# Optimization experiments

Measured on AMD Instinct MI355X. Metric: run time of the kernel, lower is better.

## Reference

```python
import jax, jax.numpy as jnp
import numpy as np

N = 4096
D_IN = 3000
D_HID = 512
D_OUT = 64
NEG_SLOPE = 0.2  # LeakyReLU alpha used by GraphAttentionLayer(.., 0.2, 0.2)
MASK_FILL = -9e15


def setup_inputs() -> dict:
    key = jax.random.key(0)
    ks = jax.random.split(key, 13)

    def p(k, shape, fan_in):
        return jax.random.normal(k, shape, dtype=jnp.float32) * np.float32(1.0 / np.sqrt(fan_in))

    return {
        "features_omics1": jax.random.normal(ks[0], (N, D_IN), dtype=jnp.float32),
        "feat_adj_omics1": jax.random.randint(ks[1], (N, N), 0, 2, dtype=jnp.int32),
        "spatial_adj_omics1": jax.random.randint(ks[2], (N, N), 0, 2, dtype=jnp.int32),
        # encoder_1: GAT(D_IN -> D_HID); encoder_2: GAT(D_HID -> D_OUT)
        "W_enc1": p(ks[3], (D_IN, D_HID), D_IN),
        "a_enc1": p(ks[4], (2 * D_HID, 1), D_HID),
        "W_enc2": p(ks[5], (D_HID, D_OUT), D_HID),
        "a_enc2": p(ks[6], (2 * D_OUT, 1), D_OUT),
        # decoder_1: GAT(D_OUT -> D_HID); decoder_2: GAT(D_HID -> D_IN)
        "W_dec1": p(ks[7], (D_OUT, D_HID), D_OUT),
        "a_dec1": p(ks[8], (2 * D_HID, 1), D_HID),
        "W_dec2": p(ks[9], (D_HID, D_IN), D_HID),
        "a_dec2": p(ks[10], (2 * D_IN, 1), D_IN),
        # AttentionLayer fusion over the two views
        "w_omega": p(ks[11], (D_OUT, D_OUT), D_OUT),
        "u_omega": p(ks[12], (D_OUT, 1), D_OUT),
    }


def _gat(h, adj, W, a):
    """Canonical dense-adjacency GAT layer (pyGAT), dropout off, ELU output."""
    Wh = h @ W                                   # [N, F]
    f = W.shape[1]
    # e[i,j] = leaky_relu(a1.Wh_i + a2.Wh_j)
    e = jax.nn.leaky_relu(Wh @ a[:f] + (Wh @ a[f:]).T, NEG_SLOPE)  # [N, N]
    att = jax.nn.softmax(jnp.where(adj > 0, e, MASK_FILL), axis=1)
    return jax.nn.elu(att @ Wh)


def _encode(x, adj, W1, a1, W2, a2):
    return _gat(_gat(x, adj, W1, a1), adj, W2, a2)


def _att_fuse(e1, e2, w_omega, u_omega):
    emb = jnp.stack([e1, e2], axis=1)            # [N, 2, D]
    v = jnp.tanh(emb @ w_omega)                  # [N, 2, D]
    vu = (v @ u_omega)[..., 0]                   # [N, 2]
    alpha = jax.nn.softmax(vu + 1e-6, axis=1)    # [N, 2]
    fused = jnp.einsum('nkd,nk->nd', emb, alpha)
    return fused, alpha


def reference(features_omics1, feat_adj_omics1, spatial_adj_omics1,
              W_enc1, a_enc1, W_enc2, a_enc2,
              W_dec1, a_dec1, W_dec2, a_dec2,
              w_omega, u_omega):
    feat_emb = _encode(features_omics1, feat_adj_omics1, W_enc1, a_enc1, W_enc2, a_enc2)
    sp_emb = _encode(features_omics1, spatial_adj_omics1, W_enc1, a_enc1, W_enc2, a_enc2)
    emb_latent, alpha = _att_fuse(feat_emb, sp_emb, w_omega, u_omega)
    recon = _gat(_gat(emb_latent, spatial_adj_omics1, W_dec1, a_dec1),
                 spatial_adj_omics1, W_dec2, a_dec2)
    corr_f = _encode(recon, feat_adj_omics1, W_enc1, a_enc1, W_enc2, a_enc2)
    corr_s = _encode(recon, spatial_adj_omics1, W_enc1, a_enc1, W_enc2, a_enc2)
    corr, _ = _att_fuse(corr_f, corr_s, w_omega, u_omega)
    return emb_latent, recon, corr, alpha
```

## Files before the change

kernel.cpp:

```cpp
#include <hip/hip_runtime.h>
#include <hip/hip_bf16.h>
#include <math.h>

using u16 = unsigned short;
using u32 = unsigned int;

typedef __attribute__((ext_vector_type(8))) short s8v;
typedef __attribute__((ext_vector_type(4))) float f4v;

__device__ __forceinline__ float bf2f(u16 u) {
    u32 x = ((u32)u) << 16;
    return __builtin_bit_cast(float, x);
}
__device__ __forceinline__ u16 f2bf(float f) {
    u32 x = __builtin_bit_cast(u32, f);
    x += 0x7fffu + ((x >> 16) & 1u);
    return (u16)(x >> 16);
}

__device__ __forceinline__ f4v mfma_bf16(s8v a, s8v b, f4v c) {
    return __builtin_amdgcn_mfma_f32_16x16x32_bf16(a, b, c, 0, 0, 0);
}

#define GLL(srcp, dstp) __builtin_amdgcn_global_load_lds( \
    (const __attribute__((address_space(1))) void*)(srcp), \
    (__attribute__((address_space(3))) void*)(dstp), 16, 0, 0)

__device__ __forceinline__ void xcd_swz(int& bx, int& by, int& bz) {
    const int nx = gridDim.x, ny = gridDim.y;
    const int total = nx * ny * gridDim.z;
    int i = (bz * ny + by) * nx + bx;
    const int q = total >> 3, r = total & 7;
    const int xcd = i & 7, k = i >> 3;
    int j = ((xcd < r) ? xcd * (q + 1) : r * (q + 1) + (xcd - r) * q) + k;
    bx = j % nx; j /= nx;
    by = j % ny;
    bz = j / ny;
}

template<bool DO_ELU, bool OUT_F32, bool OUT_SPLIT>
__global__ __launch_bounds__(256) void tgemm(
    const u16* __restrict__ A, const u16* __restrict__ Bt,
    void* __restrict__ Cv, int M, int N, int K,
    u16* __restrict__ Sh, u16* __restrict__ Sl, int Cp)
{
    constexpr int BM = 128, BN = 64, BK = 64;
    __shared__ __align__(16) u16 As[2][BM * BK];
    __shared__ __align__(16) u16 Bs[2][BN * BK];

    int bx = blockIdx.x, by = blockIdx.y, bz = blockIdx.z;
    xcd_swz(bx, by, bz);
    const int bm0 = by * BM, bn0 = bx * BN;
    const int tid = threadIdx.x;
    const int lane = tid & 63;
    const int wave = tid >> 6;
    const int wr = wave >> 1, wc = wave & 1;
    const int lr = lane & 15;
    const int srow = lane >> 3, schk = lane & 7;

    f4v acc[4][2] = {};

    auto stage = [&](int buf, int k0) {
#pragma unroll
        for (int ci = 0; ci < 4; ci++) {
            const int r8 = (wave * 4 + ci) * 8;
            const int row = r8 + srow;
            const int gchk = schk ^ (row & 7);
            GLL(A + (size_t)(bm0 + row) * K + k0 + gchk * 8, &As[buf][r8 * 64]);
        }
#pragma unroll
        for (int ci = 0; ci < 2; ci++) {
            const int r8 = (wave * 2 + ci) * 8;
            const int row = r8 + srow;
            int gn = bn0 + row;
            if (gn >= N) gn = N - 1;
            const int gchk = schk ^ (row & 7);
            GLL(Bt + (size_t)gn * K + k0 + gchk * 8, &Bs[buf][r8 * 64]);
        }
    };

    stage(0, 0);
    __syncthreads();
    int cur = 0;
    for (int k0 = 0; k0 < K; k0 += BK) {
        if (k0 + BK < K) stage(cur ^ 1, k0 + BK);
#pragma unroll
        for (int kk = 0; kk < 2; kk++) {
            const int cbase = (lane >> 4) + kk * 4;
            s8v a[4], b[2];
#pragma unroll
            for (int m = 0; m < 4; m++) {
                const int row = wr * 64 + m * 16 + lr;
                a[m] = *(const s8v*)&As[cur][row * 64 + (cbase ^ (row & 7)) * 8];
            }
#pragma unroll
            for (int n = 0; n < 2; n++) {
                const int row = wc * 32 + n * 16 + lr;
                b[n] = *(const s8v*)&Bs[cur][row * 64 + (cbase ^ (row & 7)) * 8];
            }
#pragma unroll
            for (int m = 0; m < 4; m++)
#pragma unroll
                for (int n = 0; n < 2; n++)
                    acc[m][n] = mfma_bf16(a[m], b[n], acc[m][n]);
        }
        __syncthreads();
        cur ^= 1;
    }

#pragma unroll
    for (int m = 0; m < 4; m++)
#pragma unroll
        for (int n = 0; n < 2; n++)
#pragma unroll
            for (int i = 0; i < 4; i++) {
                int gm = bm0 + wr * 64 + m * 16 + (lane >> 4) * 4 + i;
                int gn = bn0 + wc * 32 + n * 16 + lr;
                if (gm < M && gn < N) {
                    float val = acc[m][n][i];
                    if (DO_ELU) val = val > 0.f ? val : expm1f(val);
                    if (OUT_F32) {
                        ((float*)Cv)[(size_t)gm * N + gn] = val;
                        if (OUT_SPLIT) {
                            u16 hv = f2bf(val);
                            Sh[(size_t)gm * Cp + gn] = hv;
                            Sl[(size_t)gm * Cp + gn] = f2bf(val - bf2f(hv));
                        }
                    } else {
                        ((u16*)Cv)[(size_t)gm * N + gn] = f2bf(val);
                    }
                }
            }
}

__global__ __launch_bounds__(256) void tgemm_skd(
    const u16* __restrict__ A, const u16* __restrict__ BtA,
    const u16* __restrict__ BtB, float* __restrict__ P,
    int M, int Mh, int N, int K, int KS)
{
    constexpr int BM = 128, BN = 64, BK = 64;
    __shared__ __align__(16) u16 As[2][BM * BK];
    __shared__ __align__(16) u16 Bs[2][BN * BK];

    int bx = blockIdx.x, by = blockIdx.y, kz = blockIdx.z;
    xcd_swz(bx, by, kz);
    const int bm0 = by * BM, bn0 = bx * BN;
    const u16* Bt = (bm0 < Mh) ? BtA : BtB;
    const int tid = threadIdx.x;
    const int lane = tid & 63;
    const int wave = tid >> 6;
    const int wr = wave >> 1, wc = wave & 1;
    const int lr = lane & 15;
    const int srow = lane >> 3, schk = lane & 7;

    f4v acc[4][2] = {};

    auto stage = [&](int buf, int k0) {
#pragma unroll
        for (int ci = 0; ci < 4; ci++) {
            const int r8 = (wave * 4 + ci) * 8;
            const int row = r8 + srow;
            const int gchk = schk ^ (row & 7);
            GLL(A + (size_t)(bm0 + row) * K + k0 + gchk * 8, &As[buf][r8 * 64]);
        }
#pragma unroll
        for (int ci = 0; ci < 2; ci++) {
            const int r8 = (wave * 2 + ci) * 8;
            const int row = r8 + srow;
            int gn = bn0 + row;
            if (gn >= N) gn = N - 1;
            const int gchk = schk ^ (row & 7);
            GLL(Bt + (size_t)gn * K + k0 + gchk * 8, &Bs[buf][r8 * 64]);
        }
    };

    const int kbeg = kz * KS, kend = kbeg + KS;
    stage(0, kbeg);
    __syncthreads();
    int cur = 0;
    for (int k0 = kbeg; k0 < kend; k0 += BK) {
        if (k0 + BK < kend) stage(cur ^ 1, k0 + BK);
#pragma unroll
        for (int kk = 0; kk < 2; kk++) {
            const int cbase = (lane >> 4) + kk * 4;
            s8v a[4], b[2];
#pragma unroll
            for (int m = 0; m < 4; m++) {
                const int row = wr * 64 + m * 16 + lr;
                a[m] = *(const s8v*)&As[cur][row * 64 + (cbase ^ (row & 7)) * 8];
            }
#pragma unroll
            for (int n = 0; n < 2; n++) {
                const int row = wc * 32 + n * 16 + lr;
                b[n] = *(const s8v*)&Bs[cur][row * 64 + (cbase ^ (row & 7)) * 8];
            }
#pragma unroll
            for (int m = 0; m < 4; m++)
#pragma unroll
                for (int n = 0; n < 2; n++)
                    acc[m][n] = mfma_bf16(a[m], b[n], acc[m][n]);
        }
        __syncthreads();
        cur ^= 1;
    }

    float* Pz = P + (size_t)kz * M * N;
#pragma unroll
    for (int m = 0; m < 4; m++)
#pragma unroll
        for (int n = 0; n < 2; n++)
#pragma unroll
            for (int i = 0; i < 4; i++) {
                int gm = bm0 + wr * 64 + m * 16 + (lane >> 4) * 4 + i;
                int gn = bn0 + wc * 32 + n * 16 + lr;
                if (gm < M && gn < N)
                    Pz[(size_t)gm * N + gn] = acc[m][n][i];
            }
}

template<bool ELU>
__global__ __launch_bounds__(256) void skred_kernel(
    const float* __restrict__ P, u16* __restrict__ out, int total, int sk)
{
    int i = blockIdx.x * 256 + threadIdx.x;
    if (i >= total) return;
    float s = 0.f;
    for (int z = 0; z < sk; z++) s += P[(size_t)z * total + i];
    if (ELU) s = s > 0.f ? s : expm1f(s);
    out[i] = f2bf(s);
}

template<bool ASP, bool SK>
__global__ __launch_bounds__(256) void tgemm2(
    const u16* __restrict__ A0, const u16* __restrict__ A1,
    const u16* __restrict__ Bt0, const u16* __restrict__ Bt1,
    void* __restrict__ Cv, int M, int N, int K, int KS)
{
    constexpr int BM = 128, BN = 64, BK = 32;
    __shared__ __align__(16) u16 As0[2][BM * BK];
    __shared__ __align__(16) u16 As1[ASP ? 2 : 1][ASP ? BM * BK : 8];
    __shared__ __align__(16) u16 Bs0[2][BN * BK];
    __shared__ __align__(16) u16 Bs1[2][BN * BK];

    int bx = blockIdx.x, by = blockIdx.y, kz = blockIdx.z;
    xcd_swz(bx, by, kz);
    const int bm0 = by * BM, bn0 = bx * BN;
    const int tid = threadIdx.x;
    const int lane = tid & 63;
    const int wave = tid >> 6;
    const int wr = wave >> 1, wc = wave & 1;
    const int lr = lane & 15;
    const int srow = lane >> 2;
    const int schk = lane & 3;

    auto swzr = [](int row) { return (row & 3) ^ ((row >> 2) & 1); };

    f4v acc[4][2] = {};

    auto stage = [&](int buf, int k0) {
#pragma unroll
        for (int ci = 0; ci < 2; ci++) {
            const int r16 = (wave * 2 + ci) * 16;
            const int row = r16 + srow;
            const int gchk = schk ^ swzr(row);
            const size_t goff = (size_t)(bm0 + row) * K + k0 + gchk * 8;
            GLL(A0 + goff, &As0[buf][r16 * 32]);
            if constexpr (ASP) GLL(A1 + goff, &As1[buf][r16 * 32]);
        }
        {
            const int r16 = wave * 16;
            const int row = r16 + srow;
            int gn = bn0 + row;
            if (gn >= N) gn = N - 1;
            const int gchk = schk ^ swzr(row);
            const size_t goff = (size_t)gn * K + k0 + gchk * 8;
            GLL(Bt0 + goff, &Bs0[buf][r16 * 32]);
            GLL(Bt1 + goff, &Bs1[buf][r16 * 32]);
        }
    };

    const int kbeg = SK ? kz * KS : 0;
    const int kend = SK ? kbeg + KS : K;
    stage(0, kbeg);
    __syncthreads();
    int cur = 0;
    for (int k0 = kbeg; k0 < kend; k0 += BK) {
        if (k0 + BK < kend) stage(cur ^ 1, k0 + BK);
        {
            const int cbase = lane >> 4;
            s8v a0[4], a1[ASP ? 4 : 1], b0[2], b1[2];
#pragma unroll
            for (int m = 0; m < 4; m++) {
                const int row = wr * 64 + m * 16 + lr;
                const int o = row * 32 + (cbase ^ swzr(row)) * 8;
                a0[m] = *(const s8v*)&As0[cur][o];
                if constexpr (ASP) a1[m] = *(const s8v*)&As1[cur][o];
            }
#pragma unroll
            for (int n = 0; n < 2; n++) {
                const int row = wc * 32 + n * 16 + lr;
                const int o = row * 32 + (cbase ^ swzr(row)) * 8;
                b0[n] = *(const s8v*)&Bs0[cur][o];
                b1[n] = *(const s8v*)&Bs1[cur][o];
            }
#pragma unroll
            for (int m = 0; m < 4; m++)
#pragma unroll
                for (int n = 0; n < 2; n++) {
                    acc[m][n] = mfma_bf16(a0[m], b0[n], acc[m][n]);
                    acc[m][n] = mfma_bf16(a0[m], b1[n], acc[m][n]);
                    if constexpr (ASP) acc[m][n] = mfma_bf16(a1[m], b0[n], acc[m][n]);
                }
        }
        __syncthreads();
        cur ^= 1;
    }

#pragma unroll
    for (int m = 0; m < 4; m++)
#pragma unroll
        for (int n = 0; n < 2; n++)
#pragma unroll
            for (int i = 0; i < 4; i++) {
                int gm = bm0 + wr * 64 + m * 16 + (lane >> 4) * 4 + i;
                int gn = bn0 + wc * 32 + n * 16 + lr;
                if (gm < M && gn < N) {
                    if (SK) ((float*)Cv)[(size_t)kz * M * N + (size_t)gm * N + gn] = acc[m][n][i];
                    else    ((u16*)Cv)[(size_t)gm * N + gn] = f2bf(acc[m][n][i]);
                }
            }
}

__global__ __launch_bounds__(256) void skredTS_kernel(
    const float* __restrict__ P, const float* __restrict__ a,
    u16* __restrict__ wh, u16* __restrict__ tA, u16* __restrict__ tB,
    float* __restrict__ s1, float* __restrict__ s2, int n, int sk)
{
    __shared__ u16 lds[64][72];
    const int rowbase = blockIdx.x * 64;
    const int t = threadIdx.x;
    const int rl = t >> 2, cg = t & 3;
    const int row = rowbase + rl;
    const size_t M2 = (size_t)2 * n;

    float v[16];
#pragma unroll
    for (int k = 0; k < 16; k++) v[k] = 0.f;
    for (int z = 0; z < sk; z++) {
        const float4* p = (const float4*)&P[((size_t)z * M2 + row) * 64 + cg * 16];
#pragma unroll
        for (int q = 0; q < 4; q++) {
            float4 x = p[q];
            v[q * 4 + 0] += x.x; v[q * 4 + 1] += x.y;
            v[q * 4 + 2] += x.z; v[q * 4 + 3] += x.w;
        }
    }
    u16 w[16];
    float p1 = 0.f, p2 = 0.f;
#pragma unroll
    for (int k = 0; k < 16; k++) {
        w[k] = f2bf(v[k]);
        float vr = bf2f(w[k]);
        int f = cg * 16 + k;
        p1 += vr * a[f];
        p2 += vr * a[64 + f];
    }
    *(s8v*)&wh[(size_t)row * 64 + cg * 16]     = *(s8v*)&w[0];
    *(s8v*)&wh[(size_t)row * 64 + cg * 16 + 8] = *(s8v*)&w[8];
    *(s8v*)&lds[rl][cg * 16]     = *(s8v*)&w[0];
    *(s8v*)&lds[rl][cg * 16 + 8] = *(s8v*)&w[8];

    p1 += __shfl_down(p1, 1); p1 += __shfl_down(p1, 2);
    p2 += __shfl_down(p2, 1); p2 += __shfl_down(p2, 2);
    if (cg == 0) { s1[row] = p1; s2[row] = p2; }
    __syncthreads();

    const bool hb = rowbase >= n;
    u16* tX = hb ? tB : tA;
    const int grow = rowbase - (hb ? n : 0);
    u16 o[16];
#pragma unroll
    for (int k = 0; k < 16; k++) o[k] = lds[cg * 16 + k][rl];
    *(s8v*)&tX[(size_t)rl * n + grow + cg * 16]     = *(s8v*)&o[0];
    *(s8v*)&tX[(size_t)rl * n + grow + cg * 16 + 8] = *(s8v*)&o[8];
}

__global__ __launch_bounds__(256) void splitA_kernel(
    const float* __restrict__ src, u16* __restrict__ hi, u16* __restrict__ lo,
    int C, int Cp)
{
    int r = blockIdx.y;
    int c = blockIdx.x * 256 + threadIdx.x;
    if (c >= Cp) return;
    float v = (c < C) ? src[(size_t)r * C + c] : 0.f;
    u16 h = f2bf(v);
    hi[(size_t)r * Cp + c] = h;
    lo[(size_t)r * Cp + c] = f2bf(v - bf2f(h));
}

__global__ __launch_bounds__(256) void splitBT_kernel(
    const float* __restrict__ src, u16* __restrict__ hi, u16* __restrict__ lo,
    int R, int C, int Rp)
{
    __shared__ float t[32][33];
    const int r0 = blockIdx.y * 32, c0 = blockIdx.x * 32;
    const int tr = threadIdx.x >> 5, tc = threadIdx.x & 31;
#pragma unroll
    for (int i = 0; i < 4; i++) {
        int r = r0 + tr + i * 8, c = c0 + tc;
        t[tr + i * 8][tc] = (r < R && c < C) ? src[(size_t)r * C + c] : 0.f;
    }
    __syncthreads();
#pragma unroll
    for (int i = 0; i < 4; i++) {
        int c = c0 + tr + i * 8, r = r0 + tc;
        if (c < C && r < Rp) {
            float v = t[tc][tr + i * 8];
            u16 h = f2bf(v);
            hi[(size_t)c * Rp + r] = h;
            lo[(size_t)c * Rp + r] = f2bf(v - bf2f(h));
        }
    }
}

__global__ __launch_bounds__(256) void tr_kernel(
    const u16* __restrict__ src, u16* __restrict__ dst, int R, int C)
{
    __shared__ u16 t[32][33];
    const int r0 = blockIdx.y * 32, c0 = blockIdx.x * 32;
    const int tr = threadIdx.x >> 5, tc = threadIdx.x & 31;
#pragma unroll
    for (int i = 0; i < 4; i++) {
        int r = r0 + tr + i * 8, c = c0 + tc;
        t[tr + i * 8][tc] = (r < R && c < C) ? src[(size_t)r * C + c] : (u16)0;
    }
    __syncthreads();
#pragma unroll
    for (int i = 0; i < 4; i++) {
        int c = c0 + tr + i * 8, r = r0 + tc;
        if (c < C && r < R) dst[(size_t)c * R + r] = t[tc][tr + i * 8];
    }
}

__device__ __forceinline__ float block_sum4(float v, float* red) {
#pragma unroll
    for (int off = 32; off; off >>= 1) v += __shfl_down(v, off);
    int w = threadIdx.x >> 6;
    if ((threadIdx.x & 63) == 0) red[w] = v;
    __syncthreads();
    float r = red[0] + red[1] + red[2] + red[3];
    __syncthreads();
    return r;
}
__device__ __forceinline__ float block_max4(float v, float* red) {
#pragma unroll
    for (int off = 32; off; off >>= 1) v = fmaxf(v, __shfl_down(v, off));
    int w = threadIdx.x >> 6;
    if ((threadIdx.x & 63) == 0) red[w] = v;
    __syncthreads();
    float r = fmaxf(fmaxf(red[0], red[1]), fmaxf(red[2], red[3]));
    __syncthreads();
    return r;
}

__global__ __launch_bounds__(256) void scores_kernel(
    const u16* __restrict__ Wh, int ld, int F, const float* __restrict__ a,
    float* __restrict__ s1, float* __restrict__ s2)
{
    __shared__ float red[4];
    int i = blockIdx.x, tid = threadIdx.x;
    float acc1 = 0.f, acc2 = 0.f;
    for (int f = tid; f < F; f += 256) {
        float w = bf2f(Wh[(size_t)i * ld + f]);
        acc1 += w * a[f];
        acc2 += w * a[F + f];
    }
    acc1 = block_sum4(acc1, red);
    acc2 = block_sum4(acc2, red);
    if (tid == 0) { s1[i] = acc1; s2[i] = acc2; }
}

__device__ __forceinline__ void att_row(
    const u32* mask, const float* s1, const float* s2, int soff,
    u16* att, int i, int n, float* red)
{
    int tid = threadIdx.x;
    float s1i = s1[soff + i];
    int j0 = tid * 16;
    u32 w = mask[(size_t)i * (n >> 5) + (j0 >> 5)];
    u32 bits = (j0 & 16) ? (w >> 16) : (w & 0xFFFFu);

    float e[16];
    float mx = -3.0e38f;
#pragma unroll
    for (int t = 0; t < 16; t++) {
        float x = s1i + s2[soff + j0 + t];
        x = x > 0.f ? x : 0.2f * x;
        e[t] = x;
        if ((bits >> t) & 1u) mx = fmaxf(mx, x);
    }
    mx = block_max4(mx, red);

    float sum = 0.f;
#pragma unroll
    for (int t = 0; t < 16; t++) {
        float pv = ((bits >> t) & 1u) ? expf(e[t] - mx) : 0.f;
        e[t] = pv;
        sum += pv;
    }
    sum = block_sum4(sum, red);
    float rinv = sum > 0.f ? 1.f / sum : 0.f;
#pragma unroll
    for (int t = 0; t < 16; t++)
        att[(size_t)i * n + j0 + t] = f2bf(e[t] * rinv);
}

__global__ __launch_bounds__(256) void att_kernel(
    const u32* __restrict__ mask, const float* __restrict__ s1,
    const float* __restrict__ s2, u16* __restrict__ att, int n)
{
    __shared__ float red[4];
    att_row(mask, s1, s2, 0, att, blockIdx.x, n, red);
}

__global__ __launch_bounds__(256) void att2_kernel(
    const u32* __restrict__ maskA, const u32* __restrict__ maskB,
    const float* __restrict__ s1, const float* __restrict__ s2, int offB,
    u16* __restrict__ attA, u16* __restrict__ attB, int n)
{
    __shared__ float red[4];
    int b = blockIdx.x;
    if (b < n) att_row(maskA, s1, s2, 0, attA, b, n, red);
    else      att_row(maskB, s1, s2, offB, attB, b - n, n, red);
}

__global__ __launch_bounds__(64) void fuse_kernel(
    const u16* __restrict__ E1, const u16* __restrict__ E2,
    const float* __restrict__ W, const float* __restrict__ U,
    float* __restrict__ fused, float* __restrict__ alpha,
    u16* __restrict__ eh, u16* __restrict__ el)
{
    __shared__ float e1[64], e2[64];
    int i = blockIdx.x, d = threadIdx.x;
    e1[d] = bf2f(E1[i * 64 + d]);
    e2[d] = bf2f(E2[i * 64 + d]);
    __syncthreads();
    float v1 = 0.f, v2 = 0.f;
#pragma unroll 8
    for (int f = 0; f < 64; f++) {
        float w = W[f * 64 + d];
        v1 += e1[f] * w;
        v2 += e2[f] * w;
    }
    v1 = tanhf(v1); v2 = tanhf(v2);
    float u = U[d];
    float p1 = v1 * u, p2 = v2 * u;
#pragma unroll
    for (int off = 32; off; off >>= 1) {
        p1 += __shfl_down(p1, off);
        p2 += __shfl_down(p2, off);
    }
    p1 = __shfl(p1, 0); p2 = __shfl(p2, 0);
    float m = fmaxf(p1, p2);
    float w1 = expf(p1 - m), w2 = expf(p2 - m);
    float a1 = w1 / (w1 + w2), a2 = w2 / (w1 + w2);
    float fv = a1 * e1[d] + a2 * e2[d];
    fused[i * 64 + d] = fv;
    if (eh != nullptr) {
        u16 hv = f2bf(fv);
        eh[i * 64 + d] = hv;
        el[i * 64 + d] = f2bf(fv - bf2f(hv));
    }
    if (alpha != nullptr && d < 2) alpha[i * 2 + d] = (d == 0 ? a1 : a2);
}

__global__ void bitpack_kernel(const int* __restrict__ adj,
                               u32* __restrict__ mask, int nwords)
{
    int w = blockIdx.x * 256 + threadIdx.x;
    if (w >= nwords) return;
    const int* src = adj + (size_t)w * 32;
    u32 m = 0;
#pragma unroll
    for (int b = 0; b < 32; b++) m |= (src[b] > 0 ? 1u : 0u) << b;
    mask[w] = m;
}

extern "C" void kernel_launch(void* const* d_in, const int* in_sizes, int n_in,
                              void* d_out, int out_size, void* d_ws, size_t ws_size,
                              hipStream_t stream)
{
    const int N = 4096, DIN = 3000, DINP = 3008, DH = 512, DO = 64;
    const float* x      = (const float*)d_in[0];
    const int*   adjF   = (const int*)d_in[1];
    const int*   adjS   = (const int*)d_in[2];
    const float* We1    = (const float*)d_in[3];
    const float* aE1    = (const float*)d_in[4];
    const float* We2    = (const float*)d_in[5];
    const float* aE2    = (const float*)d_in[6];
    const float* Wd1    = (const float*)d_in[7];
    const float* aD1    = (const float*)d_in[8];
    const float* Wd2    = (const float*)d_in[9];
    const float* aD2    = (const float*)d_in[10];
    const float* Womega = (const float*)d_in[11];
    const float* Uomega = (const float*)d_in[12];

    float* out       = (float*)d_out;
    float* out_emb   = out;
    float* out_recon = out + (size_t)N * DO;
    float* out_corr  = out_recon + (size_t)N * DIN;
    float* out_alpha = out_corr + (size_t)N * DO;

    char* ws = (char*)d_ws;
    size_t off = 0;
    auto alloc = [&](size_t bytes) {
        size_t o = off; off += (bytes + 255) & ~(size_t)255; return o;
    };
    const size_t o_att   = alloc((size_t)2 * N * N * 2);
    const size_t o_maskF = alloc((size_t)N * (N / 32) * 4);
    const size_t o_maskS = alloc((size_t)N * (N / 32) * 4);
    const size_t o_s1    = alloc((size_t)2 * N * 4);
    const size_t o_s2    = alloc((size_t)2 * N * 4);
    const size_t o_wh1   = alloc((size_t)N * DH * 2);
    const size_t o_h1    = alloc((size_t)2 * N * DH * 2);
    const size_t o_whd1  = alloc((size_t)N * DH * 2);
    const size_t o_d1    = alloc((size_t)N * DH * 2);
    const size_t o_whd2  = alloc((size_t)N * DIN * 2);
    const size_t o_wh2   = alloc((size_t)2 * N * DO * 2);
    const size_t o_h2    = alloc((size_t)2 * N * DO * 2);
    const size_t o_t512  = alloc((size_t)DH * N * 2);
    const size_t o_td1   = alloc((size_t)DH * N * 2);
    const size_t o_td2   = alloc((size_t)DIN * N * 2);
    const size_t o_t64a  = alloc((size_t)DO * N * 2);
    const size_t o_t64b  = alloc((size_t)DO * N * 2);
    const size_t o_xh    = alloc((size_t)N * DINP * 2);
    const size_t o_xl    = alloc((size_t)N * DINP * 2);
    const size_t o_we1th = alloc((size_t)DH * DINP * 2);
    const size_t o_we1tl = alloc((size_t)DH * DINP * 2);
    const size_t o_we2th = alloc((size_t)DO * DH * 2);
    const size_t o_we2tl = alloc((size_t)DO * DH * 2);
    const size_t o_wd1th = alloc((size_t)DH * DO * 2);
    const size_t o_wd1tl = alloc((size_t)DH * DO * 2);
    const size_t o_wd2th = alloc((size_t)DIN * DH * 2);
    const size_t o_wd2tl = alloc((size_t)DIN * DH * 2);
    const size_t o_eh    = alloc((size_t)N * DO * 2);
    const size_t o_el    = alloc((size_t)N * DO * 2);
    const size_t o_skp   = alloc((size_t)8 * 2 * N * DO * 4);

    u16* attF   = (u16*)(ws + o_att);
    u16* attS   = attF + (size_t)N * N;
    u32* maskF  = (u32*)(ws + o_maskF);
    u32* maskS  = (u32*)(ws + o_maskS);
    float* s1   = (float*)(ws + o_s1);
    float* s2   = (float*)(ws + o_s2);
    u16* wh1x   = (u16*)(ws + o_wh1);
    u16* whc1   = (u16*)(ws + o_wh1);
    u16* h1     = (u16*)(ws + o_h1);
    u16* whd1   = (u16*)(ws + o_whd1);
    u16* d1b    = (u16*)(ws + o_d1);
    u16* whd2   = (u16*)(ws + o_whd2);
    u16* wh2    = (u16*)(ws + o_wh2);
    u16* h2     = (u16*)(ws + o_h2);
    u16* h2f    = h2;
    u16* h2s    = h2 + (size_t)N * DO;
    u16* t512   = (u16*)(ws + o_t512);
    u16* td1    = (u16*)(ws + o_td1);
    u16* td2    = (u16*)(ws + o_td2);
    u16* t64a   = (u16*)(ws + o_t64a);
    u16* t64b   = (u16*)(ws + o_t64b);
    u16* xh     = (u16*)(ws + o_xh);
    u16* xl     = (u16*)(ws + o_xl);
    u16* we1th  = (u16*)(ws + o_we1th);
    u16* we1tl  = (u16*)(ws + o_we1tl);
    u16* we2th  = (u16*)(ws + o_we2th);
    u16* we2tl  = (u16*)(ws + o_we2tl);
    u16* wd1th  = (u16*)(ws + o_wd1th);
    u16* wd1tl  = (u16*)(ws + o_wd1tl);
    u16* wd2th  = (u16*)(ws + o_wd2th);
    u16* wd2tl  = (u16*)(ws + o_wd2tl);
    u16* eh     = (u16*)(ws + o_eh);
    u16* el     = (u16*)(ws + o_el);
    float* skp  = (float*)(ws + o_skp);

    auto grid64 = [](int M, int Nn) { return dim3((Nn + 63) / 64, (M + 127) / 128); };
    auto tr = [&](const u16* src, u16* dst, int R, int C) {
        tr_kernel<<<dim3((C + 31) / 32, (R + 31) / 32), 256, 0, stream>>>(src, dst, R, C);
    };
    auto scores = [&](const u16* Wh, int ld, int F, const float* a) {
        scores_kernel<<<N, 256, 0, stream>>>(Wh, ld, F, a, s1, s2);
    };
    auto layer2 = [&](const u16* Astacked, u16* wh2buf, u16* h2out) {
        tgemm2<false, true><<<dim3(1, 64, 8), 256, 0, stream>>>(
            Astacked, nullptr, we2th, we2tl, skp, 2 * N, DO, DH, 64);
        skredTS_kernel<<<2 * N / 64, 256, 0, stream>>>(
            skp, aE2, wh2buf, t64a, t64b, s1, s2, N, 8);
        att2_kernel<<<2 * N, 256, 0, stream>>>(
            maskF, maskS, s1, s2, N, attF, attS, N);
        tgemm_skd<<<dim3(1, 64, 8), 256, 0, stream>>>(
            attF, t64a, t64b, skp, 2 * N, N, DO, N, 512);
        skred_kernel<true><<<(2 * N * DO + 255) / 256, 256, 0, stream>>>(
            skp, h2out, 2 * N * DO, 8);
    };

    bitpack_kernel<<<(N * (N / 32) + 255) / 256, 256, 0, stream>>>(adjF, maskF, N * (N / 32));
    bitpack_kernel<<<(N * (N / 32) + 255) / 256, 256, 0, stream>>>(adjS, maskS, N * (N / 32));
    splitA_kernel<<<dim3((DINP + 255) / 256, N), 256, 0, stream>>>(x, xh, xl, DIN, DINP);
    splitBT_kernel<<<dim3((DH + 31) / 32, (DINP + 31) / 32), 256, 0, stream>>>(We1, we1th, we1tl, DIN, DH, DINP);
    splitBT_kernel<<<dim3((DO + 31) / 32, (DH + 31) / 32), 256, 0, stream>>>(We2, we2th, we2tl, DH, DO, DH);
    splitBT_kernel<<<dim3((DH + 31) / 32, (DO + 31) / 32), 256, 0, stream>>>(Wd1, wd1th, wd1tl, DO, DH, DO);
    splitBT_kernel<<<dim3((DIN + 31) / 32, (DH + 31) / 32), 256, 0, stream>>>(Wd2, wd2th, wd2tl, DH, DIN, DH);

    tgemm2<true, false><<<grid64(N, DH), 256, 0, stream>>>(
        xh, xl, we1th, we1tl, wh1x, N, DH, DINP, DINP);
    tr(wh1x, t512, N, DH);
    scores(wh1x, DH, DH, aE1);
    att2_kernel<<<2 * N, 256, 0, stream>>>(maskF, maskS, s1, s2, 0, attF, attS, N);
    tgemm<true, false, false><<<grid64(2 * N, DH), 256, 0, stream>>>(
        attF, t512, h1, 2 * N, DH, N, nullptr, nullptr, 0);

    layer2(h1, wh2, h2);

    fuse_kernel<<<N, 64, 0, stream>>>(h2f, h2s, Womega, Uomega, out_emb, out_alpha, eh, el);

    tgemm2<true, false><<<grid64(N, DH), 256, 0, stream>>>(
        eh, el, wd1th, wd1tl, whd1, N, DH, DO, DO);
    tr(whd1, td1, N, DH);
    scores(whd1, DH, DH, aD1);
    att_kernel<<<N, 256, 0, stream>>>(maskS, s1, s2, attS, N);
    tgemm<true, false, false><<<grid64(N, DH), 256, 0, stream>>>(
        attS, td1, d1b, N, DH, N, nullptr, nullptr, 0);

    tgemm2<false, false><<<grid64(N, DIN), 256, 0, stream>>>(
        d1b, nullptr, wd2th, wd2tl, whd2, N, DIN, DH, DH);
    tr(whd2, td2, N, DIN);
    scores(whd2, DIN, DIN, aD2);
    att_kernel<<<N, 256, 0, stream>>>(maskS, s1, s2, attS, N);
    tgemm<true, true, true><<<grid64(N, DIN), 256, 0, stream>>>(
        attS, td2, out_recon, N, DIN, N, xh, xl, DINP);

    tgemm2<true, false><<<grid64(N, DH), 256, 0, stream>>>(
        xh, xl, we1th, we1tl, whc1, N, DH, DINP, DINP);
    tr(whc1, t512, N, DH);
    scores(whc1, DH, DH, aE1);
    att2_kernel<<<2 * N, 256, 0, stream>>>(maskF, maskS, s1, s2, 0, attF, attS, N);
    tgemm<true, false, false><<<grid64(2 * N, DH), 256, 0, stream>>>(
        attF, t512, h1, 2 * N, DH, N, nullptr, nullptr, 0);

    layer2(h1, wh2, h2);

    fuse_kernel<<<N, 64, 0, stream>>>(h2f, h2s, Womega, Uomega, out_corr, nullptr, nullptr, nullptr);
}
```

Before: 992.0 us.

## Fuse transposes into GEMM epilogues and split-K reduction into fuse kernel

The projection GEMMs now write a transposed bf16 copy of their output directly from the epilogue, which removes the separate transpose kernels. The split-K reduction plus ELU for layer 2 moves into the attention-fusion kernel, which removes the skred kernel and the intermediate h2 buffer. The unused Wh2 store in skredTS is dropped. The transposed stores are 8-byte strided writes, so they may be poorly coalesced compared with the tiled transpose they replace, and the fuse kernel now reads 8 fp32 partials per element.

```diff
diff --git a/kernel.cpp b/kernel.cpp
--- a/kernel.cpp
+++ b/kernel.cpp
@@ -6,6 +6,7 @@
 using u32 = unsigned int;
 
 typedef __attribute__((ext_vector_type(8))) short s8v;
+typedef __attribute__((ext_vector_type(4))) short s4v;
 typedef __attribute__((ext_vector_type(4))) float f4v;
 
 __device__ __forceinline__ float bf2f(u16 u) {
@@ -218,23 +219,12 @@
             }
 }
 
-template<bool ELU>
-__global__ __launch_bounds__(256) void skred_kernel(
-    const float* __restrict__ P, u16* __restrict__ out, int total, int sk)
-{
-    int i = blockIdx.x * 256 + threadIdx.x;
-    if (i >= total) return;
-    float s = 0.f;
-    for (int z = 0; z < sk; z++) s += P[(size_t)z * total + i];
-    if (ELU) s = s > 0.f ? s : expm1f(s);
-    out[i] = f2bf(s);
-}
-
-template<bool ASP, bool SK>
+template<bool ASP, bool SK, bool TROUT>
 __global__ __launch_bounds__(256) void tgemm2(
     const u16* __restrict__ A0, const u16* __restrict__ A1,
     const u16* __restrict__ Bt0, const u16* __restrict__ Bt1,
-    void* __restrict__ Cv, int M, int N, int K, int KS)
+    void* __restrict__ Cv, int M, int N, int K, int KS,
+    u16* __restrict__ Ct)
 {
     constexpr int BM = 128, BN = 64, BK = 32;
     __shared__ __align__(16) u16 As0[2][BM * BK];
@@ -319,21 +309,33 @@
 #pragma unroll
     for (int m = 0; m < 4; m++)
 #pragma unroll
-        for (int n = 0; n < 2; n++)
+        for (int n = 0; n < 2; n++) {
+            const int gm0 = bm0 + wr * 64 + m * 16 + (lane >> 4) * 4;
+            const int gn = bn0 + wc * 32 + n * 16 + lr;
+            u16 q[4];
 #pragma unroll
             for (int i = 0; i < 4; i++) {
-                int gm = bm0 + wr * 64 + m * 16 + (lane >> 4) * 4 + i;
-                int gn = bn0 + wc * 32 + n * 16 + lr;
+                int gm = gm0 + i;
                 if (gm < M && gn < N) {
-                    if (SK) ((float*)Cv)[(size_t)kz * M * N + (size_t)gm * N + gn] = acc[m][n][i];
-                    else    ((u16*)Cv)[(size_t)gm * N + gn] = f2bf(acc[m][n][i]);
+                    if (SK) {
+                        ((float*)Cv)[(size_t)kz * M * N + (size_t)gm * N + gn] = acc[m][n][i];
+                    } else {
+                        u16 hv = f2bf(acc[m][n][i]);
+                        ((u16*)Cv)[(size_t)gm * N + gn] = hv;
+                        q[i] = hv;
+                    }
                 }
             }
+            if constexpr (TROUT) {
+                if (gn < N && gm0 + 3 < M)
+                    *(s4v*)&Ct[(size_t)gn * M + gm0] = *(const s4v*)q;
+            }
+        }
 }
 
 __global__ __launch_bounds__(256) void skredTS_kernel(
     const float* __restrict__ P, const float* __restrict__ a,
-    u16* __restrict__ wh, u16* __restrict__ tA, u16* __restrict__ tB,
+    u16* __restrict__ tA, u16* __restrict__ tB,
     float* __restrict__ s1, float* __restrict__ s2, int n, int sk)
 {
     __shared__ u16 lds[64][72];
@@ -365,8 +367,6 @@
         p1 += vr * a[f];
         p2 += vr * a[64 + f];
     }
-    *(s8v*)&wh[(size_t)row * 64 + cg * 16]     = *(s8v*)&w[0];
-    *(s8v*)&wh[(size_t)row * 64 + cg * 16 + 8] = *(s8v*)&w[8];
     *(s8v*)&lds[rl][cg * 16]     = *(s8v*)&w[0];
     *(s8v*)&lds[rl][cg * 16 + 8] = *(s8v*)&w[8];
 
@@ -423,25 +423,6 @@
     }
 }
 
-__global__ __launch_bounds__(256) void tr_kernel(
-    const u16* __restrict__ src, u16* __restrict__ dst, int R, int C)
-{
-    __shared__ u16 t[32][33];
-    const int r0 = blockIdx.y * 32, c0 = blockIdx.x * 32;
-    const int tr = threadIdx.x >> 5, tc = threadIdx.x & 31;
-#pragma unroll
-    for (int i = 0; i < 4; i++) {
-        int r = r0 + tr + i * 8, c = c0 + tc;
-        t[tr + i * 8][tc] = (r < R && c < C) ? src[(size_t)r * C + c] : (u16)0;
-    }
-    __syncthreads();
-#pragma unroll
-    for (int i = 0; i < 4; i++) {
-        int c = c0 + tr + i * 8, r = r0 + tc;
-        if (c < C && r < R) dst[(size_t)c * R + r] = t[tc][tr + i * 8];
-    }
-}
-
 __device__ __forceinline__ float block_sum4(float v, float* red) {
 #pragma unroll
     for (int off = 32; off; off >>= 1) v += __shfl_down(v, off);
@@ -534,16 +515,24 @@
     else      att_row(maskB, s1, s2, offB, attB, b - n, n, red);
 }
 
-__global__ __launch_bounds__(64) void fuse_kernel(
-    const u16* __restrict__ E1, const u16* __restrict__ E2,
-    const float* __restrict__ W, const float* __restrict__ U,
-    float* __restrict__ fused, float* __restrict__ alpha,
-    u16* __restrict__ eh, u16* __restrict__ el)
+__global__ __launch_bounds__(64) void fuse_sk_kernel(
+    const float* __restrict__ P, const float* __restrict__ W,
+    const float* __restrict__ U, float* __restrict__ fused,
+    float* __restrict__ alpha, u16* __restrict__ eh, u16* __restrict__ el,
+    int n, int sk)
 {
     __shared__ float e1[64], e2[64];
     int i = blockIdx.x, d = threadIdx.x;
-    e1[d] = bf2f(E1[i * 64 + d]);
-    e2[d] = bf2f(E2[i * 64 + d]);
+    const size_t M2 = (size_t)2 * n;
+    float sf = 0.f, ss = 0.f;
+    for (int z = 0; z < sk; z++) {
+        sf += P[((size_t)z * M2 + i) * 64 + d];
+        ss += P[((size_t)z * M2 + n + i) * 64 + d];
+    }
+    sf = sf > 0.f ? sf : expm1f(sf);
+    ss = ss > 0.f ? ss : expm1f(ss);
+    e1[d] = sf;
+    e2[d] = ss;
     __syncthreads();
     float v1 = 0.f, v2 = 0.f;
 #pragma unroll 8
@@ -626,8 +615,6 @@
     const size_t o_whd1  = alloc((size_t)N * DH * 2);
     const size_t o_d1    = alloc((size_t)N * DH * 2);
     const size_t o_whd2  = alloc((size_t)N * DIN * 2);
-    const size_t o_wh2   = alloc((size_t)2 * N * DO * 2);
-    const size_t o_h2    = alloc((size_t)2 * N * DO * 2);
     const size_t o_t512  = alloc((size_t)DH * N * 2);
     const size_t o_td1   = alloc((size_t)DH * N * 2);
     const size_t o_td2   = alloc((size_t)DIN * N * 2);
@@ -659,10 +646,6 @@
     u16* whd1   = (u16*)(ws + o_whd1);
     u16* d1b    = (u16*)(ws + o_d1);
     u16* whd2   = (u16*)(ws + o_whd2);
-    u16* wh2    = (u16*)(ws + o_wh2);
-    u16* h2     = (u16*)(ws + o_h2);
-    u16* h2f    = h2;
-    u16* h2s    = h2 + (size_t)N * DO;
     u16* t512   = (u16*)(ws + o_t512);
     u16* td1    = (u16*)(ws + o_td1);
     u16* td2    = (u16*)(ws + o_td2);
@@ -683,23 +666,18 @@
     float* skp  = (float*)(ws + o_skp);
 
     auto grid64 = [](int M, int Nn) { return dim3((Nn + 63) / 64, (M + 127) / 128); };
-    auto tr = [&](const u16* src, u16* dst, int R, int C) {
-        tr_kernel<<<dim3((C + 31) / 32, (R + 31) / 32), 256, 0, stream>>>(src, dst, R, C);
-    };
     auto scores = [&](const u16* Wh, int ld, int F, const float* a) {
         scores_kernel<<<N, 256, 0, stream>>>(Wh, ld, F, a, s1, s2);
     };
-    auto layer2 = [&](const u16* Astacked, u16* wh2buf, u16* h2out) {
-        tgemm2<false, true><<<dim3(1, 64, 8), 256, 0, stream>>>(
-            Astacked, nullptr, we2th, we2tl, skp, 2 * N, DO, DH, 64);
+    auto layer2 = [&](const u16* Astacked) {
+        tgemm2<false, true, false><<<dim3(1, 64, 8), 256, 0, stream>>>(
+            Astacked, nullptr, we2th, we2tl, skp, 2 * N, DO, DH, 64, nullptr);
         skredTS_kernel<<<2 * N / 64, 256, 0, stream>>>(
-            skp, aE2, wh2buf, t64a, t64b, s1, s2, N, 8);
+            skp, aE2, t64a, t64b, s1, s2, N, 8);
         att2_kernel<<<2 * N, 256, 0, stream>>>(
             maskF, maskS, s1, s2, N, attF, attS, N);
         tgemm_skd<<<dim3(1, 64, 8), 256, 0, stream>>>(
             attF, t64a, t64b, skp, 2 * N, N, DO, N, 512);
-        skred_kernel<true><<<(2 * N * DO + 255) / 256, 256, 0, stream>>>(
-            skp, h2out, 2 * N * DO, 8);
     };
 
     bitpack_kernel<<<(N * (N / 32) + 255) / 256, 256, 0, stream>>>(adjF, maskF, N * (N / 32));
@@ -710,43 +688,39 @@
     splitBT_kernel<<<dim3((DH + 31) / 32, (DO + 31) / 32), 256, 0, stream>>>(Wd1, wd1th, wd1tl, DO, DH, DO);
     splitBT_kernel<<<dim3((DIN + 31) / 32, (DH + 31) / 32), 256, 0, stream>>>(Wd2, wd2th, wd2tl, DH, DIN, DH);
 
-    tgemm2<true, false><<<grid64(N, DH), 256, 0, stream>>>(
-        xh, xl, we1th, we1tl, wh1x, N, DH, DINP, DINP);
-    tr(wh1x, t512, N, DH);
+    tgemm2<true, false, true><<<grid64(N, DH), 256, 0, stream>>>(
+        xh, xl, we1th, we1tl, wh1x, N, DH, DINP, DINP, t512);
     scores(wh1x, DH, DH, aE1);
     att2_kernel<<<2 * N, 256, 0, stream>>>(maskF, maskS, s1, s2, 0, attF, attS, N);
     tgemm<true, false, false><<<grid64(2 * N, DH), 256, 0, stream>>>(
         attF, t512, h1, 2 * N, DH, N, nullptr, nullptr, 0);
 
-    layer2(h1, wh2, h2);
-
-    fuse_kernel<<<N, 64, 0, stream>>>(h2f, h2s, Womega, Uomega, out_emb, out_alpha, eh, el);
-
-    tgemm2<true, false><<<grid64(N, DH), 256, 0, stream>>>(
-        eh, el, wd1th, wd1tl, whd1, N, DH, DO, DO);
-    tr(whd1, td1, N, DH);
+    layer2(h1);
+    fuse_sk_kernel<<<N, 64, 0, stream>>>(
+        skp, Womega, Uomega, out_emb, out_alpha, eh, el, N, 8);
+
+    tgemm2<true, false, true><<<grid64(N, DH), 256, 0, stream>>>(
+        eh, el, wd1th, wd1tl, whd1, N, DH, DO, DO, td1);
     scores(whd1, DH, DH, aD1);
     att_kernel<<<N, 256, 0, stream>>>(maskS, s1, s2, attS, N);
     tgemm<true, false, false><<<grid64(N, DH), 256, 0, stream>>>(
         attS, td1, d1b, N, DH, N, nullptr, nullptr, 0);
 
-    tgemm2<false, false><<<grid64(N, DIN), 256, 0, stream>>>(
-        d1b, nullptr, wd2th, wd2tl, whd2, N, DIN, DH, DH);
-    tr(whd2, td2, N, DIN);
+    tgemm2<false, false, true><<<grid64(N, DIN), 256, 0, stream>>>(
+        d1b, nullptr, wd2th, wd2tl, whd2, N, DIN, DH, DH, td2);
     scores(whd2, DIN, DIN, aD2);
     att_kernel<<<N, 256, 0, stream>>>(maskS, s1, s2, attS, N);
     tgemm<true, true, true><<<grid64(N, DIN), 256, 0, stream>>>(
         attS, td2, out_recon, N, DIN, N, xh, xl, DINP);
 
-    tgemm2<true, false><<<grid64(N, DH), 256, 0, stream>>>(
-        xh, xl, we1th, we1tl, whc1, N, DH, DINP, DINP);
-    tr(whc1, t512, N, DH);
+    tgemm2<true, false, true><<<grid64(N, DH), 256, 0, stream>>>(
+        xh, xl, we1th, we1tl, whc1, N, DH, DINP, DINP, t512);
     scores(whc1, DH, DH, aE1);
     att2_kernel<<<2 * N, 256, 0, stream>>>(maskF, maskS, s1, s2, 0, attF, attS, N);
     tgemm<true, false, false><<<grid64(2 * N, DH), 256, 0, stream>>>(
         attF, t512, h1, 2 * N, DH, N, nullptr, nullptr, 0);
 
-    layer2(h1, wh2, h2);
-
-    fuse_kernel<<<N, 64, 0, stream>>>(h2f, h2s, Womega, Uomega, out_corr, nullptr, nullptr, nullptr);
-}
+    layer2(h1);
+    fuse_sk_kernel<<<N, 64, 0, stream>>>(
+        skp, Womega, Uomega, out_corr, nullptr, nullptr, nullptr, N, 8);
+}
```

After: 972.6 us. No clear change (-1.9%).
